# Performance work log

Measured on AMD Instinct MI355X. Metric: run time of the kernel, lower is better.

The kernel has to match this reference:

```python
import jax, jax.numpy as jnp
import numpy as np

N = 100000   # nodes
E = 1600000  # edges (avg degree 16)
Q = 64       # mesoscale velocity bins
H = 64       # collision MLP hidden dim
DT = 0.1
REG = 1e-6


def setup_inputs() -> dict:
    key = jax.random.key(0)
    ks = jax.random.split(key, 10)
    return {
        "f": jax.random.uniform(ks[0], (N, Q), jnp.float32),
        "macro_u": jax.random.normal(ks[1], (N, 1), jnp.float32),
        "source": 0.01 * jax.random.normal(ks[2], (N, Q), jnp.float32),
        "edge_src": jax.random.randint(ks[3], (E,), 0, N, jnp.int32),
        "edge_dst": jax.random.randint(ks[4], (E,), 0, N, jnp.int32),
        "edge_w": jax.random.uniform(ks[5], (E,), jnp.float32),
        "xi": jnp.linspace(-1.0, 1.0, Q).astype(jnp.float32),
        "w_in": jax.random.normal(ks[6], (Q, H), jnp.float32) / np.float32(np.sqrt(Q)),
        "b_in": jnp.zeros((H,), jnp.float32),
        "w_hid": jax.random.normal(ks[7], (3, H, H), jnp.float32) / np.float32(np.sqrt(H)),
        "b_hid": jnp.zeros((3, H), jnp.float32),
        "w_out": jax.random.normal(ks[8], (H, Q), jnp.float32) / np.float32(np.sqrt(H)),
        "b_out": jnp.zeros((Q,), jnp.float32),
    }


def _collision(f, macro_u, xi, w_in, b_in, w_hid, b_hid, w_out, b_out):
    # 5-layer MLP: relu hidden, tanh output (CollisionOperator.forward)
    x = jax.nn.relu(f @ w_in + b_in)
    for i in range(3):  # fixed small layer count, not a data-dim loop
        x = jax.nn.relu(x @ w_hid[i] + b_hid[i])
    omega = jnp.tanh(x @ w_out + b_out)                     # [N, Q]
    # Hard collision-invariance constraint: Omega* = (I - C^T (C C^T)^-1 C) Omega
    q = f.shape[1]
    w = jnp.full((q,), 1.0 / q, f.dtype)                    # quadrature weights
    xi_shifted = xi[None, :] + macro_u                      # [N, Q]
    C = jnp.stack([jnp.broadcast_to(w, xi_shifted.shape), w * xi_shifted], axis=1)  # [N,2,Q]
    CCT = jnp.einsum('naq,nbq->nab', C, C) + REG * jnp.eye(2, dtype=f.dtype)        # [N,2,2]
    v = jnp.einsum('naq,nq->na', C, omega)                  # [N,2]
    s = jnp.linalg.solve(CCT, v[..., None])[..., 0]         # [N,2]  (== CCT^-1 v)
    return omega - jnp.einsum('naq,na->nq', C, s)           # avoid dense [N,Q,Q] projection


def _transport(f, xi, edge_src, edge_dst, edge_w, n):
    # BoltzmannUpdater.compute_transport_term: both inflow (on graph) and
    # outflow (on reverse graph) reduce to the same per-edge message
    #   m_e = (w_e / out_deg[src_e]) * xi * (f[dst_e] - f[src_e])
    # aggregated at dst (inflow) and at src (outflow); transport = outflow - inflow.
    out_deg = jax.ops.segment_sum(jnp.ones_like(edge_w), edge_src, num_segments=n)
    q_e = edge_w / out_deg[edge_src]                         # [E]
    msg = q_e[:, None] * xi[None, :] * (f[edge_dst] - f[edge_src])  # [E, Q]
    inflow = jax.ops.segment_sum(msg, edge_dst, num_segments=n)
    outflow = jax.ops.segment_sum(msg, edge_src, num_segments=n)
    return outflow - inflow


def reference(f, macro_u, source, edge_src, edge_dst, edge_w, xi,
              w_in, b_in, w_hid, b_hid, w_out, b_out):
    f = jnp.maximum(f, 0.0)  # clamp(min=0)
    omega = _collision(f, macro_u, xi, w_in, b_in, w_hid, b_hid, w_out, b_out)
    trans = _transport(f, xi, edge_src, edge_dst, edge_w, f.shape[0])
    f_new = f - DT * (trans - omega - source)
    return jnp.maximum(f_new, 0.0)
```

## Files before the change

kernel.cpp:

```cpp
#include <hip/hip_runtime.h>

#define NN 100000
#define EE 1600000
#define DTc 0.1f
#define REGc 1e-6f
#define WQc (1.0f / 64.0f)

#define NB 782
#define CAP 4736
#define BS_NB 782
#define ACT_S 72
#define PRE_NB 3125
#define WP_NB 80
#define SIDE_BIT (1u << 24)

typedef unsigned long long u64;
typedef __attribute__((ext_vector_type(8))) short short8;
typedef __attribute__((ext_vector_type(4))) float f32x4;

__device__ __forceinline__ unsigned short f2bf(float x) {
    unsigned u = __float_as_uint(x);
    unsigned r = (u + 0x7fffu + ((u >> 16) & 1u)) >> 16;
    return (unsigned short)r;
}
__device__ __forceinline__ float bf2f(unsigned short s) {
    return __uint_as_float(((unsigned)s) << 16);
}
__device__ __forceinline__ unsigned pack2(float a, float b) {
    return (unsigned)f2bf(fmaxf(a, 0.f)) | ((unsigned)f2bf(fmaxf(b, 0.f)) << 16);
}

__global__ __launch_bounds__(256) void prep_kernel(
    const float* __restrict__ f, unsigned int* __restrict__ fb16u,
    const float* __restrict__ w_in, const float* __restrict__ w_hid,
    const float* __restrict__ w_out, unsigned short* __restrict__ wp,
    const int* __restrict__ esrc, const int* __restrict__ edst,
    const float* __restrict__ ew, int* __restrict__ bcur,
    u64* __restrict__ adj64) {
    int b = blockIdx.x;
    if (b < BS_NB) {
        __shared__ int cnt[NB];
        __shared__ int bas[NB];
        int t = threadIdx.x;
        for (int j = t; j < NB; j += 256) cnt[j] = 0;
        __syncthreads();
        int base = b * 2048;
        int nE = min(2048, EE - base);
        int i = t * 8;
        bool act = (i < nE);
        int4 sa, sb, da, db;
        float4 wa, wb;
        if (act) {
            sa = *(const int4*)&esrc[base + i];
            sb = *(const int4*)&esrc[base + i + 4];
            da = *(const int4*)&edst[base + i];
            db = *(const int4*)&edst[base + i + 4];
            wa = *(const float4*)&ew[base + i];
            wb = *(const float4*)&ew[base + i + 4];
            atomicAdd(&cnt[sa.x >> 7], 1); atomicAdd(&cnt[da.x >> 7], 1);
            atomicAdd(&cnt[sa.y >> 7], 1); atomicAdd(&cnt[da.y >> 7], 1);
            atomicAdd(&cnt[sa.z >> 7], 1); atomicAdd(&cnt[da.z >> 7], 1);
            atomicAdd(&cnt[sa.w >> 7], 1); atomicAdd(&cnt[da.w >> 7], 1);
            atomicAdd(&cnt[sb.x >> 7], 1); atomicAdd(&cnt[db.x >> 7], 1);
            atomicAdd(&cnt[sb.y >> 7], 1); atomicAdd(&cnt[db.y >> 7], 1);
            atomicAdd(&cnt[sb.z >> 7], 1); atomicAdd(&cnt[db.z >> 7], 1);
            atomicAdd(&cnt[sb.w >> 7], 1); atomicAdd(&cnt[db.w >> 7], 1);
        }
        __syncthreads();
        for (int j = t; j < NB; j += 256) {
            int c = cnt[j];
            bas[j] = (c ? atomicAdd(&bcur[j], c) : 0) + j * CAP;
            cnt[j] = 0;
        }
        __syncthreads();
        if (act) {
#define EMIT(s, d, w)                                                         \
            {                                                                 \
                u64 wb64 = ((u64)__float_as_uint(w)) << 32;                   \
                int p1 = bas[(s) >> 7] + atomicAdd(&cnt[(s) >> 7], 1);        \
                adj64[p1] = wb64 | SIDE_BIT | (unsigned)((d) | (((s) & 127) << 17)); \
                int p2 = bas[(d) >> 7] + atomicAdd(&cnt[(d) >> 7], 1);        \
                adj64[p2] = wb64 | (unsigned)((s) | (((d) & 127) << 17));     \
            }
            EMIT(sa.x, da.x, wa.x) EMIT(sa.y, da.y, wa.y)
            EMIT(sa.z, da.z, wa.z) EMIT(sa.w, da.w, wa.w)
            EMIT(sb.x, db.x, wb.x) EMIT(sb.y, db.y, wb.y)
            EMIT(sb.z, db.z, wb.z) EMIT(sb.w, db.w, wb.w)
#undef EMIT
        }
    } else if (b < BS_NB + PRE_NB) {
        int i = (b - BS_NB) * 256 + threadIdx.x;
        float4 v0 = *(const float4*)&f[i * 8];
        float4 v1 = *(const float4*)&f[i * 8 + 4];
        uint4 w;
        w.x = pack2(v0.x, v0.y);
        w.y = pack2(v0.z, v0.w);
        w.z = pack2(v1.x, v1.y);
        w.w = pack2(v1.z, v1.w);
        *(uint4*)&fb16u[i * 4] = w;
    } else {
        int i = (b - BS_NB - PRE_NB) * 256 + threadIdx.x;
        int l = i >> 12, idx = i & 4095;
        int n = idx >> 6, k = idx & 63;
        const float* W = (l == 0) ? w_in : (l < 4 ? w_hid + (l - 1) * 4096 : w_out);
        wp[i] = f2bf(W[k * 64 + n]);
    }
}

__global__ __launch_bounds__(256) void bucket_histo(
    const int* __restrict__ bcur, const u64* __restrict__ adj64,
    int* __restrict__ node_offs, int* __restrict__ node_end,
    int* __restrict__ deg) {
    __shared__ int cnt_tot[128], cnt_src[128], sc[128];
    int t = threadIdx.x, b = blockIdx.x;
    if (t < 128) { cnt_tot[t] = 0; cnt_src[t] = 0; }
    __syncthreads();
    int used = bcur[b];
    int gstart = b * CAP;
    for (int i = t; i < used; i += 256) {
        unsigned lo = (unsigned)adj64[gstart + i];
        int local = (lo >> 17) & 127;
        atomicAdd(&cnt_tot[local], 1);
        if (lo & SIDE_BIT) atomicAdd(&cnt_src[local], 1);
    }
    __syncthreads();
    if (t < 128) sc[t] = cnt_tot[t];
    __syncthreads();
    for (int o = 1; o < 128; o <<= 1) {
        int x = 0;
        if (t < 128 && t >= o) x = sc[t - o];
        __syncthreads();
        if (t < 128) sc[t] += x;
        __syncthreads();
    }
    if (t < 128) {
        int n = b * 128 + t;
        if (n < NN) {
            node_offs[n] = gstart + sc[t] - cnt_tot[t];
            node_end[n]  = gstart + sc[t];
            deg[n] = cnt_src[t];
        }
    }
}

__global__ __launch_bounds__(256) void bucket_scatter(
    const int* __restrict__ bcur, const u64* __restrict__ adj64,
    const int* __restrict__ node_offs, const int* __restrict__ deg,
    unsigned int* __restrict__ adj4) {
    __shared__ int cur[128];
    __shared__ float ldeg[128];
    int t = threadIdx.x, b = blockIdx.x;
    if (t < 128) {
        int n = b * 128 + t;
        cur[t] = (n < NN) ? node_offs[n] : 0;
        ldeg[t] = (n < NN) ? (float)deg[n] : 1.f;
    }
    __syncthreads();
    int used = bcur[b];
    int gstart = b * CAP;
    for (int i = t; i < used; i += 256) {
        u64 e = adj64[gstart + i];
        unsigned lo = (unsigned)e;
        int local = (lo >> 17) & 127;
        unsigned other = lo & 0x1FFFFu;
        float w = __uint_as_float((unsigned)(e >> 32));
        float dv = (lo & SIDE_BIT) ? ldeg[local] : (float)deg[other];
        float q = w / dv;
        unsigned q15 = (unsigned)(q * 32768.f + 0.5f);
        if (q15 > 32767u) q15 = 32767u;
        int p = atomicAdd(&cur[local], 1);
        adj4[p] = (q15 << 17) | other;
    }
}

#define ACC8(q, r)                                          \
    a0 = fmaf(q, __uint_as_float(r.x << 16), a0);           \
    a1 = fmaf(q, __uint_as_float(r.x & 0xFFFF0000u), a1);   \
    a2 = fmaf(q, __uint_as_float(r.y << 16), a2);           \
    a3 = fmaf(q, __uint_as_float(r.y & 0xFFFF0000u), a3);   \
    a4 = fmaf(q, __uint_as_float(r.z << 16), a4);           \
    a5 = fmaf(q, __uint_as_float(r.z & 0xFFFF0000u), a5);   \
    a6 = fmaf(q, __uint_as_float(r.w << 16), a6);           \
    a7 = fmaf(q, __uint_as_float(r.w & 0xFFFF0000u), a7);   \
    qs += q;

__global__ __launch_bounds__(256) void gather_kernel(
    const unsigned int* __restrict__ fb16u, const int* __restrict__ node_offs,
    const int* __restrict__ node_end,
    const unsigned int* __restrict__ adj, const float* __restrict__ xi,
    float* __restrict__ trans) {
    const float QS = 1.f / 32768.f;
    int lane = threadIdx.x & 63;
    int n = blockIdx.x * 4 + (threadIdx.x >> 6);
    if (n >= NN) return;
    int c = lane & 7;
    int qt = lane >> 3;
    int j = node_offs[n];
    int end = node_end[n];
    float a0 = 0.f, a1 = 0.f, a2 = 0.f, a3 = 0.f;
    float a4 = 0.f, a5 = 0.f, a6 = 0.f, a7 = 0.f, qs = 0.f;
    for (; j + 32 <= end; j += 32) {
        unsigned e0 = __builtin_nontemporal_load(&adj[j + qt]);
        unsigned e1 = __builtin_nontemporal_load(&adj[j + 8 + qt]);
        unsigned e2 = __builtin_nontemporal_load(&adj[j + 16 + qt]);
        unsigned e3 = __builtin_nontemporal_load(&adj[j + 24 + qt]);
        uint4 r0 = *(const uint4*)&fb16u[(e0 & 0x1FFFFu) * 32 + c * 4];
        uint4 r1 = *(const uint4*)&fb16u[(e1 & 0x1FFFFu) * 32 + c * 4];
        uint4 r2 = *(const uint4*)&fb16u[(e2 & 0x1FFFFu) * 32 + c * 4];
        uint4 r3 = *(const uint4*)&fb16u[(e3 & 0x1FFFFu) * 32 + c * 4];
        float q0 = (float)(e0 >> 17) * QS;
        float q1 = (float)(e1 >> 17) * QS;
        float q2 = (float)(e2 >> 17) * QS;
        float q3 = (float)(e3 >> 17) * QS;
        ACC8(q0, r0)
        ACC8(q1, r1)
        ACC8(q2, r2)
        ACC8(q3, r3)
    }
    for (; j + 8 <= end; j += 8) {
        unsigned e = __builtin_nontemporal_load(&adj[j + qt]);
        uint4 r = *(const uint4*)&fb16u[(e & 0x1FFFFu) * 32 + c * 4];
        float q = (float)(e >> 17) * QS;
        ACC8(q, r)
    }
    if (j < end) {
        int idx = j + qt;
        bool ok = idx < end;
        unsigned e = ok ? adj[idx] : 0u;
        uint4 r = *(const uint4*)&fb16u[(e & 0x1FFFFu) * 32 + c * 4];
        float q = ok ? (float)(e >> 17) * QS : 0.f;
        ACC8(q, r)
    }
#define RED3(x) x += __shfl_xor(x, 8); x += __shfl_xor(x, 16); x += __shfl_xor(x, 32)
    RED3(a0); RED3(a1); RED3(a2); RED3(a3);
    RED3(a4); RED3(a5); RED3(a6); RED3(a7); RED3(qs);
    if (qt == 0) {
        uint4 rn = *(const uint4*)&fb16u[n * 32 + c * 4];
        float4 x0 = *(const float4*)&xi[c * 8];
        float4 x1 = *(const float4*)&xi[c * 8 + 4];
        f32x4 o0, o1;
        o0.x = x0.x * (a0 - qs * __uint_as_float(rn.x << 16));
        o0.y = x0.y * (a1 - qs * __uint_as_float(rn.x & 0xFFFF0000u));
        o0.z = x0.z * (a2 - qs * __uint_as_float(rn.y << 16));
        o0.w = x0.w * (a3 - qs * __uint_as_float(rn.y & 0xFFFF0000u));
        o1.x = x1.x * (a4 - qs * __uint_as_float(rn.z << 16));
        o1.y = x1.y * (a5 - qs * __uint_as_float(rn.z & 0xFFFF0000u));
        o1.z = x1.z * (a6 - qs * __uint_as_float(rn.w << 16));
        o1.w = x1.w * (a7 - qs * __uint_as_float(rn.w & 0xFFFF0000u));
        __builtin_nontemporal_store(o0, (f32x4*)&trans[n * 64 + c * 8]);
        __builtin_nontemporal_store(o1, (f32x4*)&trans[n * 64 + c * 8 + 4]);
    }
}

__global__ __launch_bounds__(256) void node_kernel(
    const unsigned short* __restrict__ fb16, const float* __restrict__ f,
    const float* __restrict__ macro_u, const float* __restrict__ source,
    const float* __restrict__ xi, const unsigned short* __restrict__ wp,
    const float* __restrict__ b_in, const float* __restrict__ b_hid,
    const float* __restrict__ b_out,
    const float* __restrict__ trans, float* __restrict__ out) {
    __shared__ __attribute__((aligned(16))) unsigned short act[128 * ACT_S];
    __shared__ float s0s[128], s1s[128], us[128], xif[64];

    const int t = threadIdx.x;
    const int wid = t >> 6;
    const int lane = t & 63;
    const int m = lane & 15;
    const int quad = lane >> 4;
    const int nodeBase = blockIdx.x * 128;
    const int gbase = nodeBase * 64;

    if (t < 128) {
        int n = nodeBase + t;
        us[t] = (n < NN) ? macro_u[n] : 0.f;
    }
    if (t < 64) xif[t] = xi[t];

#pragma unroll
    for (int i = 0; i < 8; i++) {
        int r = wid * 32 + i * 4 + (lane >> 4);
        int c = (lane & 15) * 4;
        uint2 v = {0u, 0u};
        if (nodeBase + r < NN) v = *(const uint2*)&fb16[gbase + r * 64 + c];
        *(uint2*)&act[r * ACT_S + c] = v;
    }

    const int rowbase = wid * 32;

    for (int l = 0; l < 5; l++) {
        const unsigned short* W = wp + l * 4096;
        const float* B = (l == 0) ? b_in : (l < 4 ? b_hid + (l - 1) * 64 : b_out);

        short8 Af[2][2], Bf[4][2];
#pragma unroll
        for (int rt = 0; rt < 2; rt++)
#pragma unroll
            for (int kk = 0; kk < 2; kk++)
                Af[rt][kk] = *(const short8*)&act[(rowbase + rt * 16 + m) * ACT_S + kk * 32 + quad * 8];
#pragma unroll
        for (int ct = 0; ct < 4; ct++)
#pragma unroll
            for (int kk = 0; kk < 2; kk++)
                Bf[ct][kk] = *(const short8*)&W[(ct * 16 + m) * 64 + kk * 32 + quad * 8];

        f32x4 acc[2][4];
#pragma unroll
        for (int rt = 0; rt < 2; rt++)
#pragma unroll
            for (int ct = 0; ct < 4; ct++) {
                acc[rt][ct] = (f32x4){0.f, 0.f, 0.f, 0.f};
                acc[rt][ct] = __builtin_amdgcn_mfma_f32_16x16x32_bf16(Af[rt][0], Bf[ct][0], acc[rt][ct], 0, 0, 0);
                acc[rt][ct] = __builtin_amdgcn_mfma_f32_16x16x32_bf16(Af[rt][1], Bf[ct][1], acc[rt][ct], 0, 0, 0);
            }

#pragma unroll
        for (int rt = 0; rt < 2; rt++)
#pragma unroll
            for (int ct = 0; ct < 4; ct++) {
                float bv = B[ct * 16 + m];
#pragma unroll
                for (int r = 0; r < 4; r++) {
                    int row = rowbase + rt * 16 + quad * 4 + r;
                    float val = acc[rt][ct][r] + bv;
                    val = (l < 4) ? fmaxf(val, 0.f) : tanhf(val);
                    act[row * ACT_S + ct * 16 + m] = f2bf(val);
                }
            }
    }
    __syncthreads();

    if (t < 128) {
        float u = us[t];
        float v0 = 0.f, v1 = 0.f, sxs2 = 0.f, sxi = 0.f;
        const short8* rp = (const short8*)&act[t * ACT_S];
#pragma unroll
        for (int c = 0; c < 8; c++) {
            short8 v = rp[c];
#pragma unroll
            for (int jj = 0; jj < 8; jj++) {
                float om = bf2f((unsigned short)v[jj]);
                float xv = xif[c * 8 + jj];
                float xs = xv + u;
                v0 += om;
                v1 += xs * om;
                sxs2 += xs * xs;
                sxi += xv;
            }
        }
        v0 *= WQc;
        v1 *= WQc;
        float c00 = WQc + REGc;
        float c01 = WQc * WQc * (sxi + 64.f * u);
        float c11 = WQc * WQc * sxs2 + REGc;
        float det = c00 * c11 - c01 * c01;
        float inv = 1.0f / det;
        s0s[t] = (c11 * v0 - c01 * v1) * inv;
        s1s[t] = (c00 * v1 - c01 * v0) * inv;
    }
    __syncthreads();

#pragma unroll
    for (int i = 0; i < 8; i++) {
        int e = (i * 256 + t) * 4;
        int nl = e >> 6;
        if (nodeBase + nl < NN) {
            int g = gbase + e;
            int c0 = e & 63;
            float4 fv = *(const float4*)&f[g];
            float4 sv = *(const float4*)&source[g];
            float4 tv = *(const float4*)&trans[g];
            float uu = us[nl];
            float sv0 = s0s[nl], sv1 = s1s[nl];
            float4 ov;
            float* ovp = (float*)&ov;
            const float* fp = (const float*)&fv;
            const float* sp = (const float*)&sv;
            const float* tp = (const float*)&tv;
#pragma unroll
            for (int jj = 0; jj < 4; jj++) {
                float om = bf2f(act[nl * ACT_S + c0 + jj]);
                float xs = xif[c0 + jj] + uu;
                float omst = om - WQc * (sv0 + xs * sv1);
                float val = fmaxf(fp[jj], 0.f) + DTc * (sp[jj] + omst - tp[jj]);
                ovp[jj] = fmaxf(val, 0.f);
            }
            *(float4*)&out[g] = ov;
        }
    }
}

extern "C" void kernel_launch(void* const* d_in, const int* in_sizes, int n_in,
                              void* d_out, int out_size, void* d_ws, size_t ws_size,
                              hipStream_t stream) {
    const float* f       = (const float*)d_in[0];
    const float* macro_u = (const float*)d_in[1];
    const float* source  = (const float*)d_in[2];
    const int*   esrc    = (const int*)d_in[3];
    const int*   edst    = (const int*)d_in[4];
    const float* ew      = (const float*)d_in[5];
    const float* xi      = (const float*)d_in[6];
    const float* w_in    = (const float*)d_in[7];
    const float* b_in    = (const float*)d_in[8];
    const float* w_hid   = (const float*)d_in[9];
    const float* b_hid   = (const float*)d_in[10];
    const float* w_out   = (const float*)d_in[11];
    const float* b_out   = (const float*)d_in[12];
    float* out = (float*)d_out;

    u64* adj64 = (u64*)d_ws;
    unsigned int* adj4 = (unsigned int*)(adj64 + (size_t)NB * CAP);
    int* deg   = (int*)(adj4 + (size_t)NB * CAP);
    int* node_offs = deg + NN;
    int* node_end  = node_offs + NN;
    int* bcur  = node_end + NN;
    float* trans = (float*)(bcur + 784);
    unsigned short* fb16 = (unsigned short*)(trans + (size_t)NN * 64);
    unsigned short* wp = fb16 + (size_t)NN * 64;

    hipMemsetAsync(bcur, 0, 784 * sizeof(int), stream);

    prep_kernel<<<BS_NB + PRE_NB + WP_NB, 256, 0, stream>>>(
        f, (unsigned int*)fb16, w_in, w_hid, w_out, wp, esrc, edst, ew, bcur, adj64);
    bucket_histo<<<NB, 256, 0, stream>>>(bcur, adj64, node_offs, node_end, deg);
    bucket_scatter<<<NB, 256, 0, stream>>>(bcur, adj64, node_offs, deg, adj4);
    gather_kernel<<<(NN + 3) / 4, 256, 0, stream>>>((const unsigned int*)fb16,
                                                    node_offs, node_end, adj4, xi, trans);
    node_kernel<<<(NN + 127) / 128, 256, 0, stream>>>(
        fb16, f, macro_u, source, xi, wp, b_in, b_hid, b_out, trans, out);
}
```

Baseline: 331.6 us.

## Fuse bucket histogram and scatter into cooperative kernel; enlarge edge binning chunks

Merges the per-bucket histogram and scatter kernels into one cooperative-launched kernel that caches bucket entries in shared memory and uses a grid sync so the scatter phase can read degrees of other buckets. This removes one launch and the second global read of the bucket array. The edge binning in prep now processes 16384 edges per block with fewer blocks, reducing global atomics on bucket counters but lowering parallelism. Bucket capacity is reduced, which raises the overflow risk for skewed buckets, and cooperative launch requires all blocks to be co-resident.

```diff
diff --git a/kernel.cpp b/kernel.cpp
--- a/kernel.cpp
+++ b/kernel.cpp
@@ -1,4 +1,7 @@
 #include <hip/hip_runtime.h>
+#include <hip/hip_cooperative_groups.h>
+
+namespace cg = cooperative_groups;
 
 #define NN 100000
 #define EE 1600000
@@ -7,8 +10,9 @@
 #define WQc (1.0f / 64.0f)
 
 #define NB 782
-#define CAP 4736
-#define BS_NB 782
+#define CAP 4608
+#define BCHUNK 16384
+#define BS_NB 98
 #define ACT_S 72
 #define PRE_NB 3125
 #define WP_NB 80
@@ -44,27 +48,25 @@
         int t = threadIdx.x;
         for (int j = t; j < NB; j += 256) cnt[j] = 0;
         __syncthreads();
-        int base = b * 2048;
-        int nE = min(2048, EE - base);
-        int i = t * 8;
-        bool act = (i < nE);
-        int4 sa, sb, da, db;
-        float4 wa, wb;
-        if (act) {
-            sa = *(const int4*)&esrc[base + i];
-            sb = *(const int4*)&esrc[base + i + 4];
-            da = *(const int4*)&edst[base + i];
-            db = *(const int4*)&edst[base + i + 4];
-            wa = *(const float4*)&ew[base + i];
-            wb = *(const float4*)&ew[base + i + 4];
-            atomicAdd(&cnt[sa.x >> 7], 1); atomicAdd(&cnt[da.x >> 7], 1);
-            atomicAdd(&cnt[sa.y >> 7], 1); atomicAdd(&cnt[da.y >> 7], 1);
-            atomicAdd(&cnt[sa.z >> 7], 1); atomicAdd(&cnt[da.z >> 7], 1);
-            atomicAdd(&cnt[sa.w >> 7], 1); atomicAdd(&cnt[da.w >> 7], 1);
-            atomicAdd(&cnt[sb.x >> 7], 1); atomicAdd(&cnt[db.x >> 7], 1);
-            atomicAdd(&cnt[sb.y >> 7], 1); atomicAdd(&cnt[db.y >> 7], 1);
-            atomicAdd(&cnt[sb.z >> 7], 1); atomicAdd(&cnt[db.z >> 7], 1);
-            atomicAdd(&cnt[sb.w >> 7], 1); atomicAdd(&cnt[db.w >> 7], 1);
+        int base = b * BCHUNK;
+        int nE = min(BCHUNK, EE - base);
+#pragma unroll
+        for (int k = 0; k < 8; k++) {
+            int i = k * 2048 + t * 8;
+            if (i < nE) {
+                int4 sa = *(const int4*)&esrc[base + i];
+                int4 sb = *(const int4*)&esrc[base + i + 4];
+                int4 da = *(const int4*)&edst[base + i];
+                int4 db = *(const int4*)&edst[base + i + 4];
+                atomicAdd(&cnt[sa.x >> 7], 1); atomicAdd(&cnt[da.x >> 7], 1);
+                atomicAdd(&cnt[sa.y >> 7], 1); atomicAdd(&cnt[da.y >> 7], 1);
+                atomicAdd(&cnt[sa.z >> 7], 1); atomicAdd(&cnt[da.z >> 7], 1);
+                atomicAdd(&cnt[sa.w >> 7], 1); atomicAdd(&cnt[da.w >> 7], 1);
+                atomicAdd(&cnt[sb.x >> 7], 1); atomicAdd(&cnt[db.x >> 7], 1);
+                atomicAdd(&cnt[sb.y >> 7], 1); atomicAdd(&cnt[db.y >> 7], 1);
+                atomicAdd(&cnt[sb.z >> 7], 1); atomicAdd(&cnt[db.z >> 7], 1);
+                atomicAdd(&cnt[sb.w >> 7], 1); atomicAdd(&cnt[db.w >> 7], 1);
+            }
         }
         __syncthreads();
         for (int j = t; j < NB; j += 256) {
@@ -73,20 +75,30 @@
             cnt[j] = 0;
         }
         __syncthreads();
-        if (act) {
+#pragma unroll
+        for (int k = 0; k < 8; k++) {
+            int i = k * 2048 + t * 8;
+            if (i < nE) {
+                int4 sa = *(const int4*)&esrc[base + i];
+                int4 sb = *(const int4*)&esrc[base + i + 4];
+                int4 da = *(const int4*)&edst[base + i];
+                int4 db = *(const int4*)&edst[base + i + 4];
+                float4 wa = *(const float4*)&ew[base + i];
+                float4 wb = *(const float4*)&ew[base + i + 4];
 #define EMIT(s, d, w)                                                         \
-            {                                                                 \
-                u64 wb64 = ((u64)__float_as_uint(w)) << 32;                   \
-                int p1 = bas[(s) >> 7] + atomicAdd(&cnt[(s) >> 7], 1);        \
-                adj64[p1] = wb64 | SIDE_BIT | (unsigned)((d) | (((s) & 127) << 17)); \
-                int p2 = bas[(d) >> 7] + atomicAdd(&cnt[(d) >> 7], 1);        \
-                adj64[p2] = wb64 | (unsigned)((s) | (((d) & 127) << 17));     \
-            }
-            EMIT(sa.x, da.x, wa.x) EMIT(sa.y, da.y, wa.y)
-            EMIT(sa.z, da.z, wa.z) EMIT(sa.w, da.w, wa.w)
-            EMIT(sb.x, db.x, wb.x) EMIT(sb.y, db.y, wb.y)
-            EMIT(sb.z, db.z, wb.z) EMIT(sb.w, db.w, wb.w)
+                {                                                             \
+                    u64 wb64 = ((u64)__float_as_uint(w)) << 32;               \
+                    int p1 = bas[(s) >> 7] + atomicAdd(&cnt[(s) >> 7], 1);    \
+                    adj64[p1] = wb64 | SIDE_BIT | (unsigned)((d) | (((s) & 127) << 17)); \
+                    int p2 = bas[(d) >> 7] + atomicAdd(&cnt[(d) >> 7], 1);    \
+                    adj64[p2] = wb64 | (unsigned)((s) | (((d) & 127) << 17)); \
+                }
+                EMIT(sa.x, da.x, wa.x) EMIT(sa.y, da.y, wa.y)
+                EMIT(sa.z, da.z, wa.z) EMIT(sa.w, da.w, wa.w)
+                EMIT(sb.x, db.x, wb.x) EMIT(sb.y, db.y, wb.y)
+                EMIT(sb.z, db.z, wb.z) EMIT(sb.w, db.w, wb.w)
 #undef EMIT
+            }
         }
     } else if (b < BS_NB + PRE_NB) {
         int i = (b - BS_NB) * 256 + threadIdx.x;
@@ -107,18 +119,22 @@
     }
 }
 
-__global__ __launch_bounds__(256) void bucket_histo(
+__global__ __launch_bounds__(256) void bucket_build(
     const int* __restrict__ bcur, const u64* __restrict__ adj64,
     int* __restrict__ node_offs, int* __restrict__ node_end,
-    int* __restrict__ deg) {
-    __shared__ int cnt_tot[128], cnt_src[128], sc[128];
+    int* __restrict__ deg, unsigned int* __restrict__ adj4) {
+    __shared__ u64 ent[CAP];
+    __shared__ int cnt_tot[128], cnt_src[128], sc[128], cur[128];
+    cg::grid_group grid = cg::this_grid();
     int t = threadIdx.x, b = blockIdx.x;
     if (t < 128) { cnt_tot[t] = 0; cnt_src[t] = 0; }
     __syncthreads();
     int used = bcur[b];
     int gstart = b * CAP;
     for (int i = t; i < used; i += 256) {
-        unsigned lo = (unsigned)adj64[gstart + i];
+        u64 e = adj64[gstart + i];
+        ent[i] = e;
+        unsigned lo = (unsigned)e;
         int local = (lo >> 17) & 127;
         atomicAdd(&cnt_tot[local], 1);
         if (lo & SIDE_BIT) atomicAdd(&cnt_src[local], 1);
@@ -135,36 +151,23 @@
     }
     if (t < 128) {
         int n = b * 128 + t;
+        int st = gstart + sc[t] - cnt_tot[t];
+        cur[t] = st;
         if (n < NN) {
-            node_offs[n] = gstart + sc[t] - cnt_tot[t];
+            node_offs[n] = st;
             node_end[n]  = gstart + sc[t];
             deg[n] = cnt_src[t];
         }
     }
-}
-
-__global__ __launch_bounds__(256) void bucket_scatter(
-    const int* __restrict__ bcur, const u64* __restrict__ adj64,
-    const int* __restrict__ node_offs, const int* __restrict__ deg,
-    unsigned int* __restrict__ adj4) {
-    __shared__ int cur[128];
-    __shared__ float ldeg[128];
-    int t = threadIdx.x, b = blockIdx.x;
-    if (t < 128) {
-        int n = b * 128 + t;
-        cur[t] = (n < NN) ? node_offs[n] : 0;
-        ldeg[t] = (n < NN) ? (float)deg[n] : 1.f;
-    }
-    __syncthreads();
-    int used = bcur[b];
-    int gstart = b * CAP;
+    __threadfence();
+    grid.sync();
     for (int i = t; i < used; i += 256) {
-        u64 e = adj64[gstart + i];
+        u64 e = ent[i];
         unsigned lo = (unsigned)e;
         int local = (lo >> 17) & 127;
         unsigned other = lo & 0x1FFFFu;
         float w = __uint_as_float((unsigned)(e >> 32));
-        float dv = (lo & SIDE_BIT) ? ldeg[local] : (float)deg[other];
+        float dv = (lo & SIDE_BIT) ? (float)cnt_src[local] : (float)deg[other];
         float q = w / dv;
         unsigned q15 = (unsigned)(q * 32768.f + 0.5f);
         if (q15 > 32767u) q15 = 32767u;
@@ -421,8 +424,14 @@
 
     prep_kernel<<<BS_NB + PRE_NB + WP_NB, 256, 0, stream>>>(
         f, (unsigned int*)fb16, w_in, w_hid, w_out, wp, esrc, edst, ew, bcur, adj64);
-    bucket_histo<<<NB, 256, 0, stream>>>(bcur, adj64, node_offs, node_end, deg);
-    bucket_scatter<<<NB, 256, 0, stream>>>(bcur, adj64, node_offs, deg, adj4);
+
+    {
+        void* args[] = {(void*)&bcur, (void*)&adj64, (void*)&node_offs,
+                        (void*)&node_end, (void*)&deg, (void*)&adj4};
+        hipLaunchCooperativeKernel((void*)bucket_build, dim3(NB), dim3(256),
+                                   args, 0, stream);
+    }
+
     gather_kernel<<<(NN + 3) / 4, 256, 0, stream>>>((const unsigned int*)fb16,
                                                     node_offs, node_end, adj4, xi, trans);
     node_kernel<<<(NN + 127) / 128, 256, 0, stream>>>(
```

Result: slower. 430.5 us (+29.8%).
